# Optimization experiments

Measured on AMD Instinct MI355X. Metric: run time of the kernel, lower is better.

Reference implementation:

```python
import jax, jax.numpy as jnp
import numpy as np
import math

NUM_HEADS = 6
HIDDEN = 384
HEAD_CH = HIDDEN // NUM_HEADS
WINDOW = 4


def _get_relative_embeddings(emb, length, window):
    # emb: (H, 2*window+1, d) -> (H, 2*length-1, d)
    pad_length = max(0, length - window - 1)
    start = max(0, window - length + 1)
    padded = jnp.pad(emb, ((0, 0), (pad_length, pad_length), (0, 0)))
    return padded[:, start:start + 2 * length - 1, :]


def _relative_to_absolute(s_rel):
    # (B, H, L, 2L-1) -> (B, H, L, L) via shift-pad trick
    B, H, L, _ = s_rel.shape
    s = jnp.pad(s_rel, ((0, 0), (0, 0), (0, 0), (0, 1)))          # (B,H,L,2L)
    s = s.reshape(B, H, L * 2 * L)
    s = jnp.pad(s, ((0, 0), (0, 0), (0, L - 1)))
    s = s.reshape(B, H, L + 1, 2 * L - 1)
    return s[:, :, :L, L - 1:]


def _absolute_to_relative(score):
    # (B, H, L, L) -> (B, H, L, 2L-1)
    B, H, L, _ = score.shape
    s = jnp.pad(score, ((0, 0), (0, 0), (0, 0), (0, L - 1)))      # (B,H,L,2L-1)
    s = s.reshape(B, H, L * (2 * L - 1))
    s = jnp.pad(s, ((0, 0), (0, 0), (L, 0)))
    s = s.reshape(B, H, L, 2 * L)
    return s[:, :, :, 1:]


def setup_inputs() -> dict:
    key = jax.random.key(0)
    ks = jax.random.split(key, 11)
    B, C, L = 8, HIDDEN, 1024
    rel_std = HEAD_CH ** -0.5
    w_std = C ** -0.5
    return {
        "x": jax.random.normal(ks[0], (B, C, L), jnp.float32),
        "wq": jax.random.normal(ks[1], (C, C), jnp.float32) * w_std,
        "bq": jax.random.normal(ks[2], (C,), jnp.float32) * 0.01,
        "wk": jax.random.normal(ks[3], (C, C), jnp.float32) * w_std,
        "bk": jax.random.normal(ks[4], (C,), jnp.float32) * 0.01,
        "wv": jax.random.normal(ks[5], (C, C), jnp.float32) * w_std,
        "bv": jax.random.normal(ks[6], (C,), jnp.float32) * 0.01,
        "wo": jax.random.normal(ks[7], (C, C), jnp.float32) * w_std,
        "bo": jax.random.normal(ks[8], (C,), jnp.float32) * 0.01,
        "emb_rel_k": jax.random.normal(ks[9], (NUM_HEADS, 2 * WINDOW + 1, HEAD_CH), jnp.float32) * rel_std,
        "emb_rel_v": jax.random.normal(ks[10], (NUM_HEADS, 2 * WINDOW + 1, HEAD_CH), jnp.float32) * rel_std,
    }


def reference(x, wq, bq, wk, bk, wv, bv, wo, bo, emb_rel_k, emb_rel_v):
    B, C, L = x.shape
    H, d = NUM_HEADS, HEAD_CH
    scale = 1.0 / math.sqrt(d)

    # 1x1 convs == channel matmuls
    q = jnp.einsum('oc,bcl->bol', wq, x) + bq[:, None]
    k = jnp.einsum('oc,bcl->bol', wk, x) + bk[:, None]
    v = jnp.einsum('oc,bcl->bol', wv, x) + bv[:, None]

    # (B, C, L) -> (B, H, L, d)  (matches view(B,H,d,L).transpose(2,3))
    q = q.reshape(B, H, d, L).transpose(0, 1, 3, 2)
    k = k.reshape(B, H, d, L).transpose(0, 1, 3, 2)
    v = v.reshape(B, H, d, L).transpose(0, 1, 3, 2)

    score = jnp.einsum('bhld,bhmd->bhlm', q, k) * scale

    rel_k = _get_relative_embeddings(emb_rel_k, L, WINDOW)   # (H, 2L-1, d)
    s_rel = jnp.einsum('bhld,hmd->bhlm', q, rel_k)           # (B,H,L,2L-1)
    score = score + _relative_to_absolute(s_rel) * scale

    p = jax.nn.softmax(score, axis=-1)
    res = jnp.einsum('bhlm,bhmd->bhld', p, v)

    rel_w = _absolute_to_relative(p)                         # (B,H,L,2L-1)
    rel_v = _get_relative_embeddings(emb_rel_v, L, WINDOW)   # (H, 2L-1, d)
    res = res + jnp.einsum('bhlm,hmd->bhld', rel_w, rel_v)

    # (B,H,L,d) -> (B, C, L)
    res = res.transpose(0, 1, 3, 2).reshape(B, C, L)
    out = jnp.einsum('oc,bcl->bol', wo, res) + bo[:, None]
    return out
```

## Files before the change

kernel.cpp:

```cpp
#include <hip/hip_runtime.h>
#include <hip/hip_bf16.h>

#define NB 8
#define CH 384
#define SL 1024
#define NH 6
#define HD 64
#define WIN 4
#define LOG2E 1.44269504088896340736f
#define SCALE 0.125f
#define QSCALE (SCALE * LOG2E)
#define SCLAMP2 14.4269504f
#define PAD 76

typedef _Float16 f16;
typedef f16   f16x8 __attribute__((ext_vector_type(8)));
typedef f16   f16x4 __attribute__((ext_vector_type(4)));
typedef float f32x4 __attribute__((ext_vector_type(4)));
typedef unsigned short u16x8 __attribute__((ext_vector_type(8)));
typedef unsigned short u16x4 __attribute__((ext_vector_type(4)));

static __device__ __forceinline__ unsigned short f2bf_rne(float f) {
  unsigned int u = __float_as_uint(f);
  unsigned int r = (u + 0x7fffu + ((u >> 16) & 1u)) >> 16;
  return (unsigned short)r;
}
static __device__ __forceinline__ float bfb(unsigned short u) {
  return __uint_as_float((unsigned int)u << 16);
}
static __device__ __forceinline__ float ldbf(const void* p, size_t i) {
  return bfb(((const unsigned short*)p)[i]);
}
static __device__ __forceinline__ float ldf(const void* p, size_t i) {
  return ((const float*)p)[i];
}
static __device__ __forceinline__ float fexp2(float x) {
  return __builtin_amdgcn_exp2f(x);
}

__global__ __launch_bounds__(256) void cvt_k(
    const void* __restrict__ w0, const void* __restrict__ w1,
    const void* __restrict__ w2, const void* __restrict__ w3,
    const void* __restrict__ b0, const void* __restrict__ b1,
    const void* __restrict__ b2, const void* __restrict__ b3,
    const void* __restrict__ x,
    f16* __restrict__ wh, float* __restrict__ bh, f16* __restrict__ xt,
    int* __restrict__ flag)
{
  __shared__ f16 lt_[64][72];
  __shared__ int sflag;
  const int bx = blockIdx.x, t = threadIdx.x;

  {
    int cnt = 0;
    if (t < 64) {
      const unsigned int* xu = (const unsigned int*)x;
#pragma unroll
      for (int i = 0; i < 4; ++i) {
        unsigned int e = (xu[t * 4 + i] >> 7) & 0xFF;
        if (e >= 110 && e <= 140) ++cnt;
      }
#pragma unroll
      for (int s = 1; s < 64; s <<= 1) cnt += __shfl_xor(cnt, s);
      if (t == 0) sflag = (cnt >= 128) ? 1 : 0;
    }
    __syncthreads();
  }
  const int isbf = sflag;

  if (bx < 576) {
    int g = bx / 144;
    const void* src = (g == 0) ? w0 : (g == 1) ? w1 : (g == 2) ? w2 : w3;
    size_t idx = (size_t)(bx % 144) * 1024 + t * 4;
    f16* dst = wh + (size_t)g * CH * CH + idx;
    f16x4 o;
    if (!isbf) {
      float4 v = *(const float4*)((const float*)src + idx);
      o[0] = (f16)v.x; o[1] = (f16)v.y; o[2] = (f16)v.z; o[3] = (f16)v.w;
    } else {
      u16x4 v = *(const u16x4*)((const unsigned short*)src + idx);
#pragma unroll
      for (int j = 0; j < 4; ++j) o[j] = (f16)bfb(v[j]);
    }
    *(f16x4*)dst = o;
    return;
  }
  if (bx == 576) {
    if (t == 0) *flag = isbf;
    for (int e = t; e < 4 * CH; e += 256) {
      int g = e / CH, i = e - g * CH;
      const void* src = (g == 0) ? b0 : (g == 1) ? b1 : (g == 2) ? b2 : b3;
      bh[e] = isbf ? ldbf(src, i) : ldf(src, i);
    }
    return;
  }
  const int e  = bx - 577;
  const int l0 = (e & 15) * 64;
  const int c0 = ((e >> 4) % 6) * 64;
  const int b  = e / 96;
  const int row = t >> 4, lseg = t & 15;

  if (!isbf) {
    const float* xf = (const float*)x;
#pragma unroll
    for (int k = 0; k < 4; ++k) {
      int c = c0 + row + 16 * k;
      float4 v = *(const float4*)&xf[((size_t)b * CH + c) * SL + l0 + lseg * 4];
      lt_[lseg * 4 + 0][row + 16 * k] = (f16)v.x;
      lt_[lseg * 4 + 1][row + 16 * k] = (f16)v.y;
      lt_[lseg * 4 + 2][row + 16 * k] = (f16)v.z;
      lt_[lseg * 4 + 3][row + 16 * k] = (f16)v.w;
    }
  } else {
    const unsigned short* xu = (const unsigned short*)x;
#pragma unroll
    for (int k = 0; k < 4; ++k) {
      int c = c0 + row + 16 * k;
      u16x4 v = *(const u16x4*)&xu[((size_t)b * CH + c) * SL + l0 + lseg * 4];
#pragma unroll
      for (int j = 0; j < 4; ++j)
        lt_[lseg * 4 + j][row + 16 * k] = (f16)bfb(v[j]);
    }
  }
  __syncthreads();
  const int l = t >> 2, seg = t & 3;
  f16* dst = &xt[((size_t)b * SL + l0 + l) * CH + c0 + seg * 16];
  *(f16x8*)dst       = *(const f16x8*)&lt_[l][seg * 16];
  *(f16x8*)(dst + 8) = *(const f16x8*)&lt_[l][seg * 16 + 8];
}

__global__ __launch_bounds__(256) void qkv_k(
    const f16* __restrict__ wh, const float* __restrict__ bh, const f16* __restrict__ xt,
    f16* __restrict__ Q, f16* __restrict__ K, f16* __restrict__ Vt)
{
  __shared__ f16 sm[2][128][PAD];

  const int t   = threadIdx.x;
  const int l0  = blockIdx.x * 128;
  const int mty = blockIdx.y;
  const int b   = blockIdx.z;
  const int wid = t >> 6, lane = t & 63;
  const int quad = lane >> 4, lid = lane & 15;
  const int rw = wid >> 1, cw = wid & 1;

  const int g0   = mty / 3;
  const int m128 = (mty % 3) * 128;
  const f16* wg  = wh + (size_t)g0 * CH * CH;

  f32x4 acc[4][4];
#pragma unroll
  for (int mt = 0; mt < 4; ++mt)
#pragma unroll
    for (int nt = 0; nt < 4; ++nt) acc[mt][nt] = (f32x4){0.f, 0.f, 0.f, 0.f};

  for (int c0 = 0; c0 < CH; c0 += 64) {
    __syncthreads();
#pragma unroll
    for (int k = 0; k < 4; ++k) {
      int cidx = t + k * 256;
      int r = cidx >> 3, c8 = (cidx & 7) * 8;
      *(f16x8*)&sm[0][r][c8] = *(const f16x8*)&wg[(size_t)(m128 + r) * CH + c0 + c8];
      *(f16x8*)&sm[1][r][c8] = *(const f16x8*)&xt[((size_t)b * SL + l0 + r) * CH + c0 + c8];
    }
    __syncthreads();
#pragma unroll
    for (int kk = 0; kk < 2; ++kk) {
      f16x8 bf[4];
#pragma unroll
      for (int nt = 0; nt < 4; ++nt)
        bf[nt] = *(const f16x8*)&sm[1][cw * 64 + nt * 16 + lid][kk * 32 + quad * 8];
#pragma unroll
      for (int mt = 0; mt < 4; ++mt) {
        f16x8 af = *(const f16x8*)&sm[0][rw * 64 + mt * 16 + lid][kk * 32 + quad * 8];
#pragma unroll
        for (int nt = 0; nt < 4; ++nt)
          acc[mt][nt] = __builtin_amdgcn_mfma_f32_16x16x32_f16(af, bf[nt], acc[mt][nt], 0, 0, 0);
      }
    }
  }
  __syncthreads();

  const int h = (mty % 3) * 2 + rw;
  float bias[4][4];
#pragma unroll
  for (int mt = 0; mt < 4; ++mt)
#pragma unroll
    for (int r = 0; r < 4; ++r)
      bias[mt][r] = bh[g0 * CH + m128 + rw * 64 + mt * 16 + quad * 4 + r];
  const float osc = (g0 == 0) ? QSCALE : 1.0f;

  f16 (*lo4)[64][PAD] = (f16(*)[64][PAD])sm;

  if (g0 < 2) {
#pragma unroll
    for (int mt = 0; mt < 4; ++mt)
#pragma unroll
      for (int nt = 0; nt < 4; ++nt) {
        f16x4 vv;
#pragma unroll
        for (int r = 0; r < 4; ++r)
          vv[r] = (f16)((acc[mt][nt][r] + bias[mt][r]) * osc);
        *(f16x4*)&lo4[wid][nt * 16 + lid][mt * 16 + quad * 4] = vv;
      }
    __builtin_amdgcn_s_waitcnt(0);
    f16* base = ((g0 == 0) ? Q : K) + ((size_t)(b * NH + h) * SL + l0 + cw * 64) * HD;
#pragma unroll
    for (int p = 0; p < 8; ++p) {
      int lr = p * 8 + (lane >> 3), seg = lane & 7;
      *(f16x8*)&base[(size_t)lr * HD + seg * 8] = *(const f16x8*)&lo4[wid][lr][seg * 8];
    }
  } else {
#pragma unroll
    for (int mt = 0; mt < 4; ++mt)
#pragma unroll
      for (int nt = 0; nt < 4; ++nt)
#pragma unroll
        for (int r = 0; r < 4; ++r)
          lo4[wid][mt * 16 + quad * 4 + r][nt * 16 + lid] =
            (f16)(acc[mt][nt][r] + bias[mt][r]);
    __builtin_amdgcn_s_waitcnt(0);
    f16* base = Vt + ((size_t)(b * NH + h) * HD) * SL + l0 + cw * 64;
#pragma unroll
    for (int p = 0; p < 8; ++p) {
      int dr = p * 8 + (lane >> 3), seg = lane & 7;
      *(f16x8*)&base[(size_t)dr * SL + seg * 8] = *(const f16x8*)&lo4[wid][dr][seg * 8];
    }
  }
}

__global__ __launch_bounds__(256) void attn_k(
    const f16* __restrict__ Qs, const f16* __restrict__ Kg, const f16* __restrict__ Vtg,
    const void* __restrict__ embk, const void* __restrict__ embv,
    f16* __restrict__ R2t, const int* __restrict__ flag)
{
  __shared__ f16 bufk[2][64][PAD];
  __shared__ f16 bufv[2][64][PAD];
  __shared__ float lbias[64][12];
  __shared__ float lsb[64][12];
  __shared__ float lev[9][64];
  __shared__ float ll64[64];

  const int isbf = *flag;
  const int t    = threadIdx.x;

  const int id   = blockIdx.x;
  const int xcd  = id & 7;
  const int kk   = id >> 3;
  const int pair = (kk % 6) * 8 + xcd;
  const int i0   = (kk / 6) * 64;
  const int b    = pair / NH;
  const int h    = pair % NH;

  const int wid  = t >> 6;
  const int lane = t & 63;
  const int quad = lane >> 4;
  const int lid  = lane & 15;

  const f16* Qb = Qs  + ((size_t)(b * NH + h) * SL) * HD;
  const f16* Kb = Kg  + ((size_t)(b * NH + h) * SL) * HD;
  const f16* Vb = Vtg + ((size_t)(b * NH + h) * HD) * SL;

  f16 (* const lq)[PAD] = bufk[0];
  f16 (* const lo)[PAD] = bufk[0];

  const int r_0 = t >> 3,         c8 = (t & 7) * 8;
  const int r_1 = (t + 256) >> 3;
  const int u0   = t & 7;
  const int jt0  = u0 >> 1;
  const int colA = ((2 * u0) & 3) * 16 + jt0 * 4;
  const int colB = ((2 * u0 + 1) & 3) * 16 + jt0 * 4;

#pragma unroll
  for (int k = 0; k < 2; ++k) {
    int c = t + k * 256, r = c >> 3, cc8 = (c & 7) * 8;
    *(f16x8*)&lq[r][cc8] = *(const f16x8*)&Qb[(size_t)(i0 + r) * HD + cc8];
  }
  f16x8 pk0 = *(const f16x8*)&Kb[(size_t)r_0 * HD + c8];
  f16x8 pk1 = *(const f16x8*)&Kb[(size_t)r_1 * HD + c8];
  f16x8 pv0 = *(const f16x8*)&Vb[(size_t)r_0 * SL + c8];
  f16x8 pv1 = *(const f16x8*)&Vb[(size_t)r_1 * SL + c8];

  for (int e = t; e < 576; e += 256) {
    int p = e >> 6, c = e & 63;
    lev[p][c] = isbf ? ldbf(embv, (size_t)h * 576 + e) : ldf(embv, (size_t)h * 576 + e);
  }
  for (int e = t; e < 768; e += 256) ((float*)lsb)[e] = -1e30f;
  __syncthreads();

  const f16x8 qf0 = *(const f16x8*)&lq[16 * wid + lid][quad * 8];
  const f16x8 qf1 = *(const f16x8*)&lq[16 * wid + lid][32 + quad * 8];

  {
    int row = h * 9 + (lid < 9 ? lid : 0);
    f16x8 ekf0, ekf1;
    if (!isbf) {
      const float* ek = (const float*)embk;
#pragma unroll
      for (int e = 0; e < 8; ++e) {
        ekf0[e] = (f16)ek[(size_t)row * HD + quad * 8 + e];
        ekf1[e] = (f16)ek[(size_t)row * HD + 32 + quad * 8 + e];
      }
    } else {
      const unsigned short* ek = (const unsigned short*)embk;
      u16x8 v0 = *(const u16x8*)&ek[(size_t)row * HD + quad * 8];
      u16x8 v1 = *(const u16x8*)&ek[(size_t)row * HD + 32 + quad * 8];
#pragma unroll
      for (int e = 0; e < 8; ++e) { ekf0[e] = (f16)bfb(v0[e]); ekf1[e] = (f16)bfb(v1[e]); }
    }
    f32x4 bd = (f32x4){0.f, 0.f, 0.f, 0.f};
    bd = __builtin_amdgcn_mfma_f32_16x16x32_f16(ekf0, qf0, bd, 0, 0, 0);
    bd = __builtin_amdgcn_mfma_f32_16x16x32_f16(ekf1, qf1, bd, 0, 0, 0);
#pragma unroll
    for (int r = 0; r < 4; ++r) {
      int p = quad * 4 + r;
      if (p < 9) lbias[16 * wid + lid][p] = bd[r];
    }
  }
  __syncthreads();

  const f16x4 ones4 = {(f16)1.f, (f16)1.f, (f16)1.f, (f16)1.f};

  f32x4 O[4];
  f32x4 Os = (f32x4){0.f, 0.f, 0.f, 0.f};
#pragma unroll
  for (int dt = 0; dt < 4; ++dt) O[dt] = (f32x4){0.f, 0.f, 0.f, 0.f};

  const int irow = 16 * wid + lid;

  int ib = 0;
  for (int j0 = 0; j0 < SL; j0 += 64, ib ^= 1) {
    *(f16x8*)&bufk[ib][r_0][c8] = pk0;
    *(f16x8*)&bufk[ib][r_1][c8] = pk1;
    *(f16x4*)&bufv[ib][r_0][colA] = __builtin_shufflevector(pv0, pv0, 0, 1, 2, 3);
    *(f16x4*)&bufv[ib][r_0][colB] = __builtin_shufflevector(pv0, pv0, 4, 5, 6, 7);
    *(f16x4*)&bufv[ib][r_1][colA] = __builtin_shufflevector(pv1, pv1, 0, 1, 2, 3);
    *(f16x4*)&bufv[ib][r_1][colB] = __builtin_shufflevector(pv1, pv1, 4, 5, 6, 7);
    __syncthreads();

    if (j0 + 64 < SL) {
      pk0 = *(const f16x8*)&Kb[(size_t)(j0 + 64 + r_0) * HD + c8];
      pk1 = *(const f16x8*)&Kb[(size_t)(j0 + 64 + r_1) * HD + c8];
      pv0 = *(const f16x8*)&Vb[(size_t)r_0 * SL + j0 + 64 + c8];
      pv1 = *(const f16x8*)&Vb[(size_t)r_1 * SL + j0 + 64 + c8];
    }

    f32x4 sc[4];
#pragma unroll
    for (int jt = 0; jt < 4; ++jt) {
      f16x8 a0 = *(const f16x8*)&bufk[ib][jt * 16 + lid][quad * 8];
      f16x8 a1 = *(const f16x8*)&bufk[ib][jt * 16 + lid][32 + quad * 8];
      f32x4 z = (f32x4){0.f, 0.f, 0.f, 0.f};
      sc[jt] = __builtin_amdgcn_mfma_f32_16x16x32_f16(a0, qf0, z, 0, 0, 0);
      sc[jt] = __builtin_amdgcn_mfma_f32_16x16x32_f16(a1, qf1, sc[jt], 0, 0, 0);
    }

    if (j0 - i0 <= 64 && i0 - j0 <= 64) {
#pragma unroll
      for (int jt = 0; jt < 4; ++jt)
#pragma unroll
        for (int r = 0; r < 4; ++r) {
          int d = (j0 + jt * 16 + quad * 4 + r) - (i0 + irow) + WIN;
          if (d >= 0 && d <= 2 * WIN) {
            float s = sc[jt][r] + lbias[irow][d];
            sc[jt][r] = s;
            lsb[irow][d] = s;
          }
        }
    }

    f16x4 pb[4];
#pragma unroll
    for (int jt = 0; jt < 4; ++jt)
#pragma unroll
      for (int r = 0; r < 4; ++r)
        pb[jt][r] = (f16)fexp2(fminf(sc[jt][r], SCLAMP2));

#pragma unroll
    for (int jt = 0; jt < 4; ++jt)
      Os = __builtin_amdgcn_mfma_f32_16x16x16f16(ones4, pb[jt], Os, 0, 0, 0);

#pragma unroll
    for (int dt = 0; dt < 4; ++dt) {
      f16x8 va01 = *(const f16x8*)&bufv[ib][dt * 16 + lid][quad * 16];
      f16x8 va23 = *(const f16x8*)&bufv[ib][dt * 16 + lid][quad * 16 + 8];
      O[dt] = __builtin_amdgcn_mfma_f32_16x16x16f16(
                __builtin_shufflevector(va01, va01, 0, 1, 2, 3), pb[0], O[dt], 0, 0, 0);
      O[dt] = __builtin_amdgcn_mfma_f32_16x16x16f16(
                __builtin_shufflevector(va01, va01, 4, 5, 6, 7), pb[1], O[dt], 0, 0, 0);
      O[dt] = __builtin_amdgcn_mfma_f32_16x16x16f16(
                __builtin_shufflevector(va23, va23, 0, 1, 2, 3), pb[2], O[dt], 0, 0, 0);
      O[dt] = __builtin_amdgcn_mfma_f32_16x16x16f16(
                __builtin_shufflevector(va23, va23, 4, 5, 6, 7), pb[3], O[dt], 0, 0, 0);
    }
  }

  if (quad == 0) ll64[irow] = Os[0];
  __syncthreads();

  for (int e = t; e < 576; e += 256) {
    int r = e / 9, p = e - r * 9;
    lsb[r][p] = fexp2(fminf(lsb[r][p], SCLAMP2)) * __builtin_amdgcn_rcpf(ll64[r]);
  }
  __syncthreads();

  {
    const float rl = __builtin_amdgcn_rcpf(Os[0]);
    float lp[9];
#pragma unroll
    for (int p = 0; p < 9; ++p) lp[p] = lsb[irow][p];
    float val[4][4];
#pragma unroll
    for (int dt = 0; dt < 4; ++dt)
#pragma unroll
      for (int r = 0; r < 4; ++r) val[dt][r] = O[dt][r] * rl;
#pragma unroll
    for (int p = 0; p < 9; ++p)
#pragma unroll
      for (int dt = 0; dt < 4; ++dt)
#pragma unroll
        for (int r = 0; r < 4; ++r)
          val[dt][r] += lp[p] * lev[p][dt * 16 + quad * 4 + r];
#pragma unroll
    for (int dt = 0; dt < 4; ++dt) {
      f16x4 vv;
#pragma unroll
      for (int r = 0; r < 4; ++r) vv[r] = (f16)val[dt][r];
      *(f16x4*)&lo[irow][dt * 16 + quad * 4] = vv;
    }
  }
  __syncthreads();

  {
    const int l = t >> 2, seg = t & 3;
    f16* dst = &R2t[((size_t)b * SL + i0 + l) * CH + h * 64 + seg * 16];
    *(f16x8*)dst       = *(const f16x8*)&lo[l][seg * 16];
    *(f16x8*)(dst + 8) = *(const f16x8*)&lo[l][seg * 16 + 8];
  }
}

__global__ __launch_bounds__(256) void out_k(
    const f16* __restrict__ wh, const float* __restrict__ bh, const f16* __restrict__ R2t,
    void* __restrict__ out, const int* __restrict__ flag)
{
  __shared__ f16 sm[2][128][PAD];

  const int isbf = *flag;
  const int t   = threadIdx.x;
  const int l0  = blockIdx.x * 128;
  const int m0  = blockIdx.y * 128;
  const int b   = blockIdx.z;
  const int wid = t >> 6, lane = t & 63;
  const int quad = lane >> 4, lid = lane & 15;
  const int rw = wid >> 1, cw = wid & 1;

  const f16* wg = wh + (size_t)3 * CH * CH;

  f32x4 acc[4][4];
#pragma unroll
  for (int mt = 0; mt < 4; ++mt)
#pragma unroll
    for (int nt = 0; nt < 4; ++nt) acc[mt][nt] = (f32x4){0.f, 0.f, 0.f, 0.f};

  for (int c0 = 0; c0 < CH; c0 += 64) {
    __syncthreads();
#pragma unroll
    for (int k = 0; k < 4; ++k) {
      int cidx = t + k * 256;
      int r = cidx >> 3, c8 = (cidx & 7) * 8;
      *(f16x8*)&sm[0][r][c8] = *(const f16x8*)&wg[(size_t)(m0 + r) * CH + c0 + c8];
      *(f16x8*)&sm[1][r][c8] = *(const f16x8*)&R2t[((size_t)b * SL + l0 + r) * CH + c0 + c8];
    }
    __syncthreads();
#pragma unroll
    for (int kk = 0; kk < 2; ++kk) {
      f16x8 bf[4];
#pragma unroll
      for (int nt = 0; nt < 4; ++nt)
        bf[nt] = *(const f16x8*)&sm[1][cw * 64 + nt * 16 + lid][kk * 32 + quad * 8];
#pragma unroll
      for (int mt = 0; mt < 4; ++mt) {
        f16x8 af = *(const f16x8*)&sm[0][rw * 64 + mt * 16 + lid][kk * 32 + quad * 8];
#pragma unroll
        for (int nt = 0; nt < 4; ++nt)
          acc[mt][nt] = __builtin_amdgcn_mfma_f32_16x16x32_f16(af, bf[nt], acc[mt][nt], 0, 0, 0);
      }
    }
  }

  float bias[4][4];
#pragma unroll
  for (int mt = 0; mt < 4; ++mt)
#pragma unroll
    for (int r = 0; r < 4; ++r)
      bias[mt][r] = bh[3 * CH + m0 + rw * 64 + mt * 16 + quad * 4 + r];

  if (isbf) {
    __syncthreads();
    unsigned short (*lo4)[64][PAD] = (unsigned short(*)[64][PAD])sm;
#pragma unroll
    for (int mt = 0; mt < 4; ++mt)
#pragma unroll
      for (int nt = 0; nt < 4; ++nt)
#pragma unroll
        for (int r = 0; r < 4; ++r)
          lo4[wid][mt * 16 + quad * 4 + r][nt * 16 + lid] =
            f2bf_rne(acc[mt][nt][r] + bias[mt][r]);
    __builtin_amdgcn_s_waitcnt(0);
    unsigned short* base = (unsigned short*)out
      + ((size_t)b * CH + m0 + rw * 64) * SL + l0 + cw * 64;
#pragma unroll
    for (int p = 0; p < 8; ++p) {
      int mr = p * 8 + (lane >> 3), seg = lane & 7;
      *(u16x8*)&base[(size_t)mr * SL + seg * 8] = *(const u16x8*)&lo4[wid][mr][seg * 8];
    }
  } else {
#pragma unroll
    for (int mt = 0; mt < 4; ++mt)
#pragma unroll
      for (int nt = 0; nt < 4; ++nt)
#pragma unroll
        for (int r = 0; r < 4; ++r) {
          int m = m0 + rw * 64 + mt * 16 + quad * 4 + r;
          int l = l0 + cw * 64 + nt * 16 + lid;
          ((float*)out)[((size_t)b * CH + m) * SL + l] = acc[mt][nt][r] + bias[mt][r];
        }
  }
}

extern "C" void kernel_launch(void* const* d_in, const int* in_sizes, int n_in,
                              void* d_out, int out_size, void* d_ws, size_t ws_size,
                              hipStream_t stream) {
  (void)in_sizes; (void)n_in; (void)out_size; (void)ws_size;
  const void* x  = d_in[0];
  const void* wq = d_in[1]; const void* bq = d_in[2];
  const void* wk = d_in[3]; const void* bk = d_in[4];
  const void* wv = d_in[5]; const void* bv = d_in[6];
  const void* wo = d_in[7]; const void* bo = d_in[8];
  const void* ek = d_in[9]; const void* ev = d_in[10];

  const size_t NQ = (size_t)NB * NH * SL * HD;
  const size_t NX = (size_t)NB * SL * CH;
  char* w = (char*)d_ws;
  int*   flag = (int*)w;                 w += 256;
  f16*   wh   = (f16*)w;                 w += 4 * CH * CH * sizeof(f16);
  float* bh   = (float*)w;               w += 4 * CH * sizeof(float);
  f16*   xt   = (f16*)w;                 w += NX * sizeof(f16);
  f16*   Q    = (f16*)w;                 w += NQ * sizeof(f16);
  f16*   K    = (f16*)w;                 w += NQ * sizeof(f16);
  f16*   Vt   = (f16*)w;                 w += NQ * sizeof(f16);
  f16*   R2t  = (f16*)w;                 w += NX * sizeof(f16);

  cvt_k   <<<1345, 256, 0, stream>>>(wq, wk, wv, wo, bq, bk, bv, bo, x, wh, bh, xt, flag);
  qkv_k   <<<dim3(8, 9, NB), 256, 0, stream>>>(wh, bh, xt, Q, K, Vt);
  attn_k  <<<768, 256, 0, stream>>>(Q, K, Vt, ek, ev, R2t, flag);
  out_k   <<<dim3(8, 3, NB), 256, 0, stream>>>(wh, bh, R2t, d_out, flag);
}
```

Measured before the change: 147.5 us.

## Split attention waves into 2x2 query/key quadrants with cross-wave reduction

Each wave now computes a 32-query by 32-key quadrant of the 64x64 tile instead of 16 queries across all 64 keys, so each K/V fragment loaded from LDS feeds two MFMAs. Partial outputs and row sums are reduced across the two key-half waves through shared memory after the loop. V is stored untransposed (no scatter), the LDS pad shrinks, custom lgkmcnt-only barriers replace __syncthreads, and launch bounds request 3 blocks per CU. The cost is more accumulator registers and an extra reduction pass at the end.

```diff
diff --git a/kernel.cpp b/kernel.cpp
--- a/kernel.cpp
+++ b/kernel.cpp
@@ -11,7 +11,7 @@
 #define SCALE 0.125f
 #define QSCALE (SCALE * LOG2E)
 #define SCLAMP2 14.4269504f
-#define PAD 76
+#define PAD 72
 
 typedef _Float16 f16;
 typedef f16   f16x8 __attribute__((ext_vector_type(8)));
@@ -37,6 +37,12 @@
 static __device__ __forceinline__ float fexp2(float x) {
   return __builtin_amdgcn_exp2f(x);
 }
+
+#define BAR() do {                                            \
+    asm volatile("s_waitcnt lgkmcnt(0)" ::: "memory");        \
+    __builtin_amdgcn_s_barrier();                             \
+    asm volatile("" ::: "memory");                            \
+  } while (0)
 
 __global__ __launch_bounds__(256) void cvt_k(
     const void* __restrict__ w0, const void* __restrict__ w1,
@@ -228,17 +234,17 @@
   }
 }
 
-__global__ __launch_bounds__(256) void attn_k(
+__global__ __launch_bounds__(256, 3) void attn_k(
     const f16* __restrict__ Qs, const f16* __restrict__ Kg, const f16* __restrict__ Vtg,
     const void* __restrict__ embk, const void* __restrict__ embv,
     f16* __restrict__ R2t, const int* __restrict__ flag)
 {
-  __shared__ f16 bufk[2][64][PAD];
-  __shared__ f16 bufv[2][64][PAD];
+  __shared__ f16 bufall[4][64][PAD];
   __shared__ float lbias[64][12];
   __shared__ float lsb[64][12];
   __shared__ float lev[9][64];
   __shared__ float ll64[64];
+  __shared__ float lred[4][2][16];
 
   const int isbf = *flag;
   const int t    = threadIdx.x;
@@ -255,20 +261,21 @@
   const int lane = t & 63;
   const int quad = lane >> 4;
   const int lid  = lane & 15;
+  const int ih   = wid >> 1;
+  const int jh   = wid & 1;
+  const int irow = 16 * wid + lid;
 
   const f16* Qb = Qs  + ((size_t)(b * NH + h) * SL) * HD;
   const f16* Kb = Kg  + ((size_t)(b * NH + h) * SL) * HD;
   const f16* Vb = Vtg + ((size_t)(b * NH + h) * HD) * SL;
 
-  f16 (* const lq)[PAD] = bufk[0];
-  f16 (* const lo)[PAD] = bufk[0];
-
-  const int r_0 = t >> 3,         c8 = (t & 7) * 8;
+  f16 (*bufk)[64][PAD] = &bufall[0];
+  f16 (*bufv)[64][PAD] = &bufall[2];
+  f16 (* const lq)[PAD] = bufall[0];
+  f16 (* const lo)[PAD] = bufall[0];
+
+  const int r_0 = t >> 3, c8 = (t & 7) * 8;
   const int r_1 = (t + 256) >> 3;
-  const int u0   = t & 7;
-  const int jt0  = u0 >> 1;
-  const int colA = ((2 * u0) & 3) * 16 + jt0 * 4;
-  const int colB = ((2 * u0 + 1) & 3) * 16 + jt0 * 4;
 
 #pragma unroll
   for (int k = 0; k < 2; ++k) {
@@ -285,10 +292,14 @@
     lev[p][c] = isbf ? ldbf(embv, (size_t)h * 576 + e) : ldf(embv, (size_t)h * 576 + e);
   }
   for (int e = t; e < 768; e += 256) ((float*)lsb)[e] = -1e30f;
-  __syncthreads();
-
-  const f16x8 qf0 = *(const f16x8*)&lq[16 * wid + lid][quad * 8];
-  const f16x8 qf1 = *(const f16x8*)&lq[16 * wid + lid][32 + quad * 8];
+  BAR();
+
+  f16x8 qn0[2], qn1[2];
+#pragma unroll
+  for (int nt = 0; nt < 2; ++nt) {
+    qn0[nt] = *(const f16x8*)&lq[ih * 32 + nt * 16 + lid][quad * 8];
+    qn1[nt] = *(const f16x8*)&lq[ih * 32 + nt * 16 + lid][32 + quad * 8];
+  }
 
   {
     int row = h * 9 + (lid < 9 ? lid : 0);
@@ -308,34 +319,34 @@
       for (int e = 0; e < 8; ++e) { ekf0[e] = (f16)bfb(v0[e]); ekf1[e] = (f16)bfb(v1[e]); }
     }
     f32x4 bd = (f32x4){0.f, 0.f, 0.f, 0.f};
-    bd = __builtin_amdgcn_mfma_f32_16x16x32_f16(ekf0, qf0, bd, 0, 0, 0);
-    bd = __builtin_amdgcn_mfma_f32_16x16x32_f16(ekf1, qf1, bd, 0, 0, 0);
+    bd = __builtin_amdgcn_mfma_f32_16x16x32_f16(ekf0, qn0[jh], bd, 0, 0, 0);
+    bd = __builtin_amdgcn_mfma_f32_16x16x32_f16(ekf1, qn1[jh], bd, 0, 0, 0);
 #pragma unroll
     for (int r = 0; r < 4; ++r) {
       int p = quad * 4 + r;
-      if (p < 9) lbias[16 * wid + lid][p] = bd[r];
-    }
-  }
-  __syncthreads();
+      if (p < 9) lbias[irow][p] = bd[r];
+    }
+  }
+  BAR();
 
   const f16x4 ones4 = {(f16)1.f, (f16)1.f, (f16)1.f, (f16)1.f};
 
-  f32x4 O[4];
-  f32x4 Os = (f32x4){0.f, 0.f, 0.f, 0.f};
-#pragma unroll
-  for (int dt = 0; dt < 4; ++dt) O[dt] = (f32x4){0.f, 0.f, 0.f, 0.f};
-
-  const int irow = 16 * wid + lid;
+  f32x4 Op[2][4];
+  f32x4 Os[2];
+#pragma unroll
+  for (int nt = 0; nt < 2; ++nt) {
+    Os[nt] = (f32x4){0.f, 0.f, 0.f, 0.f};
+#pragma unroll
+    for (int dt = 0; dt < 4; ++dt) Op[nt][dt] = (f32x4){0.f, 0.f, 0.f, 0.f};
+  }
 
   int ib = 0;
   for (int j0 = 0; j0 < SL; j0 += 64, ib ^= 1) {
     *(f16x8*)&bufk[ib][r_0][c8] = pk0;
     *(f16x8*)&bufk[ib][r_1][c8] = pk1;
-    *(f16x4*)&bufv[ib][r_0][colA] = __builtin_shufflevector(pv0, pv0, 0, 1, 2, 3);
-    *(f16x4*)&bufv[ib][r_0][colB] = __builtin_shufflevector(pv0, pv0, 4, 5, 6, 7);
-    *(f16x4*)&bufv[ib][r_1][colA] = __builtin_shufflevector(pv1, pv1, 0, 1, 2, 3);
-    *(f16x4*)&bufv[ib][r_1][colB] = __builtin_shufflevector(pv1, pv1, 4, 5, 6, 7);
-    __syncthreads();
+    *(f16x8*)&bufv[ib][r_0][c8] = pv0;
+    *(f16x8*)&bufv[ib][r_1][c8] = pv1;
+    BAR();
 
     if (j0 + 64 < SL) {
       pk0 = *(const f16x8*)&Kb[(size_t)(j0 + 64 + r_0) * HD + c8];
@@ -344,57 +355,89 @@
       pv1 = *(const f16x8*)&Vb[(size_t)r_1 * SL + j0 + 64 + c8];
     }
 
-    f32x4 sc[4];
-#pragma unroll
-    for (int jt = 0; jt < 4; ++jt) {
-      f16x8 a0 = *(const f16x8*)&bufk[ib][jt * 16 + lid][quad * 8];
-      f16x8 a1 = *(const f16x8*)&bufk[ib][jt * 16 + lid][32 + quad * 8];
+    f16x8 a00 = *(const f16x8*)&bufk[ib][jh * 32 + lid][quad * 8];
+    f16x8 a10 = *(const f16x8*)&bufk[ib][jh * 32 + lid][32 + quad * 8];
+    f16x8 a01 = *(const f16x8*)&bufk[ib][jh * 32 + 16 + lid][quad * 8];
+    f16x8 a11 = *(const f16x8*)&bufk[ib][jh * 32 + 16 + lid][32 + quad * 8];
+
+    f32x4 sc[2][2];
+#pragma unroll
+    for (int nt = 0; nt < 2; ++nt) {
       f32x4 z = (f32x4){0.f, 0.f, 0.f, 0.f};
-      sc[jt] = __builtin_amdgcn_mfma_f32_16x16x32_f16(a0, qf0, z, 0, 0, 0);
-      sc[jt] = __builtin_amdgcn_mfma_f32_16x16x32_f16(a1, qf1, sc[jt], 0, 0, 0);
+      sc[0][nt] = __builtin_amdgcn_mfma_f32_16x16x32_f16(a00, qn0[nt], z, 0, 0, 0);
+      sc[0][nt] = __builtin_amdgcn_mfma_f32_16x16x32_f16(a10, qn1[nt], sc[0][nt], 0, 0, 0);
+      sc[1][nt] = __builtin_amdgcn_mfma_f32_16x16x32_f16(a01, qn0[nt], z, 0, 0, 0);
+      sc[1][nt] = __builtin_amdgcn_mfma_f32_16x16x32_f16(a11, qn1[nt], sc[1][nt], 0, 0, 0);
     }
 
     if (j0 - i0 <= 64 && i0 - j0 <= 64) {
 #pragma unroll
-      for (int jt = 0; jt < 4; ++jt)
-#pragma unroll
-        for (int r = 0; r < 4; ++r) {
-          int d = (j0 + jt * 16 + quad * 4 + r) - (i0 + irow) + WIN;
-          if (d >= 0 && d <= 2 * WIN) {
-            float s = sc[jt][r] + lbias[irow][d];
-            sc[jt][r] = s;
-            lsb[irow][d] = s;
+      for (int jt = 0; jt < 2; ++jt)
+#pragma unroll
+        for (int nt = 0; nt < 2; ++nt)
+#pragma unroll
+          for (int r = 0; r < 4; ++r) {
+            int jl = jh * 32 + jt * 16 + quad * 4 + r;
+            int il = ih * 32 + nt * 16 + lid;
+            int d = (j0 + jl) - (i0 + il) + WIN;
+            if (d >= 0 && d <= 2 * WIN) {
+              float s = sc[jt][nt][r] + lbias[il][d];
+              sc[jt][nt][r] = s;
+              lsb[il][d] = s;
+            }
           }
-        }
-    }
-
-    f16x4 pb[4];
-#pragma unroll
-    for (int jt = 0; jt < 4; ++jt)
-#pragma unroll
-      for (int r = 0; r < 4; ++r)
-        pb[jt][r] = (f16)fexp2(fminf(sc[jt][r], SCLAMP2));
-
-#pragma unroll
-    for (int jt = 0; jt < 4; ++jt)
-      Os = __builtin_amdgcn_mfma_f32_16x16x16f16(ones4, pb[jt], Os, 0, 0, 0);
+    }
+
+    f16x4 pb[2][2];
+#pragma unroll
+    for (int jt = 0; jt < 2; ++jt)
+#pragma unroll
+      for (int nt = 0; nt < 2; ++nt)
+#pragma unroll
+        for (int r = 0; r < 4; ++r)
+          pb[jt][nt][r] = (f16)fexp2(fminf(sc[jt][nt][r], SCLAMP2));
+
+#pragma unroll
+    for (int nt = 0; nt < 2; ++nt) {
+      Os[nt] = __builtin_amdgcn_mfma_f32_16x16x16f16(ones4, pb[0][nt], Os[nt], 0, 0, 0);
+      Os[nt] = __builtin_amdgcn_mfma_f32_16x16x16f16(ones4, pb[1][nt], Os[nt], 0, 0, 0);
+    }
 
 #pragma unroll
     for (int dt = 0; dt < 4; ++dt) {
-      f16x8 va01 = *(const f16x8*)&bufv[ib][dt * 16 + lid][quad * 16];
-      f16x8 va23 = *(const f16x8*)&bufv[ib][dt * 16 + lid][quad * 16 + 8];
-      O[dt] = __builtin_amdgcn_mfma_f32_16x16x16f16(
-                __builtin_shufflevector(va01, va01, 0, 1, 2, 3), pb[0], O[dt], 0, 0, 0);
-      O[dt] = __builtin_amdgcn_mfma_f32_16x16x16f16(
-                __builtin_shufflevector(va01, va01, 4, 5, 6, 7), pb[1], O[dt], 0, 0, 0);
-      O[dt] = __builtin_amdgcn_mfma_f32_16x16x16f16(
-                __builtin_shufflevector(va23, va23, 0, 1, 2, 3), pb[2], O[dt], 0, 0, 0);
-      O[dt] = __builtin_amdgcn_mfma_f32_16x16x16f16(
-                __builtin_shufflevector(va23, va23, 4, 5, 6, 7), pb[3], O[dt], 0, 0, 0);
-    }
-  }
-
-  if (quad == 0) ll64[irow] = Os[0];
+      f16x4 vf0 = *(const f16x4*)&bufv[ib][dt * 16 + lid][jh * 32 + quad * 4];
+      f16x4 vf1 = *(const f16x4*)&bufv[ib][dt * 16 + lid][jh * 32 + 16 + quad * 4];
+#pragma unroll
+      for (int nt = 0; nt < 2; ++nt) {
+        Op[nt][dt] = __builtin_amdgcn_mfma_f32_16x16x16f16(vf0, pb[0][nt], Op[nt][dt], 0, 0, 0);
+        Op[nt][dt] = __builtin_amdgcn_mfma_f32_16x16x16f16(vf1, pb[1][nt], Op[nt][dt], 0, 0, 0);
+      }
+    }
+  }
+
+  __syncthreads();
+  float* red = (float*)bufall;
+#pragma unroll
+  for (int nt = 0; nt < 2; ++nt)
+#pragma unroll
+    for (int dt = 0; dt < 4; ++dt)
+      *(f32x4*)&red[(((wid * 2 + nt) * 4 + dt) * 64 + lane) * 4] = Op[nt][dt];
+  if (quad == 0) {
+    lred[wid][0][lid] = Os[0][0];
+    lred[wid][1][lid] = Os[1][0];
+  }
+  __syncthreads();
+
+  const int u0w = (wid >> 1) * 2, u1w = u0w + 1, ntw = wid & 1;
+  f32x4 O[4];
+#pragma unroll
+  for (int dt = 0; dt < 4; ++dt) {
+    f32x4 xA = *(const f32x4*)&red[(((u0w * 2 + ntw) * 4 + dt) * 64 + lane) * 4];
+    f32x4 xB = *(const f32x4*)&red[(((u1w * 2 + ntw) * 4 + dt) * 64 + lane) * 4];
+    O[dt] = xA + xB;
+  }
+  const float lsum = lred[u0w][ntw][lid] + lred[u1w][ntw][lid];
+  if (quad == 0) ll64[irow] = lsum;
   __syncthreads();
 
   for (int e = t; e < 576; e += 256) {
@@ -404,7 +447,7 @@
   __syncthreads();
 
   {
-    const float rl = __builtin_amdgcn_rcpf(Os[0]);
+    const float rl = __builtin_amdgcn_rcpf(lsum);
     float lp[9];
 #pragma unroll
     for (int p = 0; p < 9; ++p) lp[p] = lsb[irow][p];
```

New measurement: 147.3 us. About the same (-0.2%).
